# Kernel optimization log

Hardware: AMD Instinct MI355X
Metric: run time of the kernel (lower is better)

Reference implementation:

```python
import jax, jax.numpy as jnp
import numpy as np

BITS = 8
CLIP_BOUND = 2.0 ** (BITS - 1) - 1.0  # 127 for int8
EPS = 1e-12


def _per_tensor_scale(x):
    # Dynamic per-tensor abs-max calibration (TensorQuantizer.update with
    # calibration over the whole tensor): scale maps abs-max to the clip bound.
    amax = jnp.max(jnp.abs(x))
    return CLIP_BOUND / jnp.maximum(amax, EPS)


def setup_inputs() -> dict:
    key = jax.random.key(0)
    k1, k2 = jax.random.split(key)
    lhs = jax.random.normal(k1, (4096, 4096), dtype=jnp.float32)
    rhs = jax.random.normal(k2, (4096, 4096), dtype=jnp.float32)
    return {"lhs": lhs, "rhs": rhs}


def reference(lhs, rhs):
    # --- calibration (scales are statistics, no gradient flows through them) ---
    ls = _per_tensor_scale(lhs)
    rs = _per_tensor_scale(rhs)

    # --- quantize to int8 grid ---
    ql = jnp.clip(jnp.round(lhs * ls), -CLIP_BOUND, CLIP_BOUND).astype(jnp.int8)
    qr = jnp.clip(jnp.round(rhs * rs), -CLIP_BOUND, CLIP_BOUND).astype(jnp.int8)

    # --- integer dot_general with int32 accumulation (aqt_dot_general core) ---
    dimension_numbers = (((1,), (0,)), ((), ()))
    acc = jax.lax.dot_general(
        ql, qr, dimension_numbers, preferred_element_type=jnp.int32
    )

    # --- dequantize by product of scales ---
    out = acc.astype(jnp.float32) / (ls * rs)
    return out
```

## Files before the change

kernel.cpp:

```cpp
#include <hip/hip_runtime.h>
#include <stdint.h>


#define NROW 4096
#define NELEM (4096 * 4096)

typedef __attribute__((ext_vector_type(4))) int int32x4;
typedef __attribute__((ext_vector_type(16))) int int32x16;
typedef const __attribute__((address_space(1))) int8_t* gptr1_t;
typedef __attribute__((address_space(3))) int8_t* lptr3_t;

__global__ void absmax_both_kernel(const float* __restrict__ lhs,
                                   const float* __restrict__ rhs,
                                   unsigned* __restrict__ amax) {
    __shared__ float red[4];
    const int t = blockIdx.x & 1;
    const float4* x4 = (const float4*)(t ? rhs : lhs);
    const int bid = blockIdx.x >> 1;
    const int stride = (gridDim.x >> 1) * blockDim.x;
    int i = bid * blockDim.x + threadIdx.x;
    float m0 = 0.0f, m1 = 0.0f, m2 = 0.0f, m3 = 0.0f;
    for (; i + 3 * stride < NELEM / 4; i += 4 * stride) {
        float4 a = x4[i];
        float4 b = x4[i + stride];
        float4 c = x4[i + 2 * stride];
        float4 d = x4[i + 3 * stride];
        m0 = fmaxf(m0, fmaxf(fmaxf(fabsf(a.x), fabsf(a.y)),
                             fmaxf(fabsf(a.z), fabsf(a.w))));
        m1 = fmaxf(m1, fmaxf(fmaxf(fabsf(b.x), fabsf(b.y)),
                             fmaxf(fabsf(b.z), fabsf(b.w))));
        m2 = fmaxf(m2, fmaxf(fmaxf(fabsf(c.x), fabsf(c.y)),
                             fmaxf(fabsf(c.z), fabsf(c.w))));
        m3 = fmaxf(m3, fmaxf(fmaxf(fabsf(d.x), fabsf(d.y)),
                             fmaxf(fabsf(d.z), fabsf(d.w))));
    }
    for (; i < NELEM / 4; i += stride) {
        float4 a = x4[i];
        m0 = fmaxf(m0, fmaxf(fmaxf(fabsf(a.x), fabsf(a.y)),
                             fmaxf(fabsf(a.z), fabsf(a.w))));
    }
    float m = fmaxf(fmaxf(m0, m1), fmaxf(m2, m3));
    for (int off = 32; off > 0; off >>= 1)
        m = fmaxf(m, __shfl_down(m, off, 64));
    const int lane = threadIdx.x & 63, wave = threadIdx.x >> 6;
    if (lane == 0) red[wave] = m;
    __syncthreads();
    if (threadIdx.x == 0) {
        float b = fmaxf(fmaxf(red[0], red[1]), fmaxf(red[2], red[3]));
        atomicMax(amax + t, __float_as_uint(b));
    }
}

__device__ __forceinline__ int q8(float v, float s) {
    int r = __float2int_rn(v * s);
    r = r < -127 ? -127 : r;
    r = r > 127 ? 127 : r;
    return r;
}

__global__ void quant_kernel(const float* __restrict__ lhs,
                             const float* __restrict__ rhs,
                             int8_t* __restrict__ qA, int8_t* __restrict__ qT,
                             const unsigned* __restrict__ amax) {
    __shared__ int8_t sm[64][68];
    if (blockIdx.x < 16384) {
        const float s = 127.0f / fmaxf(__uint_as_float(amax[0]), 1e-12f);
        const int i = blockIdx.x * blockDim.x + threadIdx.x;
        float4 v = ((const float4*)lhs)[i];
        int b0 = q8(v.x, s), b1 = q8(v.y, s), b2 = q8(v.z, s), b3 = q8(v.w, s);
        ((int*)qA)[i] = (b0 & 0xff) | ((b1 & 0xff) << 8) | ((b2 & 0xff) << 16)
                      | ((b3 & 0xff) << 24);
    } else {
        const float s = 127.0f / fmaxf(__uint_as_float(amax[1]), 1e-12f);
        const int b = blockIdx.x - 16384;
        const int n0 = (b & 63) * 64, k0 = (b >> 6) * 64;
        const int rl = threadIdx.x >> 4;
        const int nq = threadIdx.x & 15;
        for (int r = 0; r < 4; ++r) {
            const int kl = r * 16 + rl;
            float4 v = *(const float4*)(rhs + (size_t)(k0 + kl) * NROW + n0 + nq * 4);
            sm[nq * 4 + 0][kl] = (int8_t)q8(v.x, s);
            sm[nq * 4 + 1][kl] = (int8_t)q8(v.y, s);
            sm[nq * 4 + 2][kl] = (int8_t)q8(v.z, s);
            sm[nq * 4 + 3][kl] = (int8_t)q8(v.w, s);
        }
        __syncthreads();
        const int nl = threadIdx.x >> 2;
        const int kq = threadIdx.x & 3;
        int4 w;
        w.x = *(const int*)&sm[nl][kq * 16 + 0];
        w.y = *(const int*)&sm[nl][kq * 16 + 4];
        w.z = *(const int*)&sm[nl][kq * 16 + 8];
        w.w = *(const int*)&sm[nl][kq * 16 + 12];
        *(int4*)(qT + (size_t)(n0 + nl) * NROW + k0 + kq * 16) = w;
    }
}

__global__ __launch_bounds__(512, 2) void gemm_i8_kernel(
    const int8_t* __restrict__ qA, const int8_t* __restrict__ qBT,
    float* __restrict__ out, const unsigned* __restrict__ amax) {
    __shared__ __align__(16) int8_t sA[2][256 * 128];
    __shared__ __align__(16) int8_t sB[2][256 * 128];

    const int tid = threadIdx.x;
    const int lane = tid & 63;
    const int wave = tid >> 6;
    const int wm = wave >> 2;
    const int wn = wave & 3;

    const int bid = blockIdx.y * 16 + blockIdx.x;
    const int swz = (bid & 7) * 32 + (bid >> 3);
    const int m0 = (swz >> 4) * 256, n0 = (swz & 15) * 256;

    const int rl = lane & 31;
    const int hi = lane >> 5;

    const int rowA = wm * 128 + rl;
    const int rowB = wn * 64 + rl;
    int aoff4[4], boff4[4];
#pragma unroll
    for (int ks = 0; ks < 4; ++ks) {
        aoff4[ks] = rowA * 128 + (((2 * ks + hi + rowA) & 7) << 4);
        boff4[ks] = rowB * 128 + (((2 * ks + hi + rowB) & 7) << 4);
    }

    gptr1_t pA[4], pB[4];
#pragma unroll
    for (int j = 0; j < 4; ++j) {
        const int c = tid + j * 512;
        const int row = c >> 3;
        const int G = ((c & 7) - row) & 7;
        pA[j] = (gptr1_t)(qA + (size_t)(m0 + row) * NROW + G * 16);
        pB[j] = (gptr1_t)(qBT + (size_t)(n0 + row) * NROW + G * 16);
    }
    int8_t* sAf = &sA[0][0];
    int8_t* sBf = &sB[0][0];
    const int dst0 = tid * 16;

    auto stage = [&](int slot, int kb) {
#pragma unroll
        for (int j = 0; j < 4; ++j) {
            __builtin_amdgcn_global_load_lds(
                pA[j] + kb, (lptr3_t)(sAf + slot * 32768 + dst0 + j * 8192),
                16, 0, 0);
            __builtin_amdgcn_global_load_lds(
                pB[j] + kb, (lptr3_t)(sBf + slot * 32768 + dst0 + j * 8192),
                16, 0, 0);
        }
    };

    int32x16 acc[4][2];
#pragma unroll
    for (int mt = 0; mt < 4; ++mt)
#pragma unroll
        for (int nt = 0; nt < 2; ++nt) acc[mt][nt] = (int32x16)(0);

    auto compute = [&](const int8_t* a, const int8_t* b) {
#pragma unroll
        for (int ks = 0; ks < 4; ++ks) {
            int32x4 af[4], bf[2];
#pragma unroll
            for (int mt = 0; mt < 4; ++mt)
                af[mt] = *(const int32x4*)(a + aoff4[ks] + mt * 4096);
#pragma unroll
            for (int nt = 0; nt < 2; ++nt)
                bf[nt] = *(const int32x4*)(b + boff4[ks] + nt * 4096);
            __builtin_amdgcn_s_setprio(1);
#pragma unroll
            for (int mt = 0; mt < 4; ++mt)
#pragma unroll
                for (int nt = 0; nt < 2; ++nt)
                    acc[mt][nt] = __builtin_amdgcn_mfma_i32_32x32x32_i8(
                        af[mt], bf[nt], acc[mt][nt], 0, 0, 0);
            __builtin_amdgcn_s_setprio(0);
        }
    };

    stage(0, 0);
    asm volatile("s_waitcnt vmcnt(0)" ::: "memory");
    __builtin_amdgcn_sched_barrier(0);
    __builtin_amdgcn_s_barrier();
    __builtin_amdgcn_sched_barrier(0);

#pragma unroll 1
    for (int w = 0; w < 31; ++w) {
        stage((w + 1) & 1, (w + 1) * 128);
        compute(sAf + (w & 1) * 32768, sBf + (w & 1) * 32768);
        asm volatile("s_waitcnt vmcnt(0)" ::: "memory");
        __builtin_amdgcn_sched_barrier(0);
        __builtin_amdgcn_s_barrier();
        __builtin_amdgcn_sched_barrier(0);
    }
    compute(sAf + 32768, sBf + 32768);

    const float ls = 127.0f / fmaxf(__uint_as_float(amax[0]), 1e-12f);
    const float rs = 127.0f / fmaxf(__uint_as_float(amax[1]), 1e-12f);
    const float inv = 1.0f / (ls * rs);
#pragma unroll
    for (int mt = 0; mt < 4; ++mt)
#pragma unroll
        for (int nt = 0; nt < 2; ++nt)
#pragma unroll
            for (int reg = 0; reg < 16; ++reg) {
                const int row = m0 + wm * 128 + mt * 32 + (reg & 3) +
                                8 * (reg >> 2) + 4 * hi;
                const int col = n0 + wn * 64 + nt * 32 + rl;
                out[(size_t)row * NROW + col] = (float)acc[mt][nt][reg] * inv;
            }
}

extern "C" void kernel_launch(void* const* d_in, const int* in_sizes, int n_in,
                              void* d_out, int out_size, void* d_ws,
                              size_t ws_size, hipStream_t stream) {
    const float* lhs = (const float*)d_in[0];
    const float* rhs = (const float*)d_in[1];
    float* out = (float*)d_out;

    int8_t* qA = (int8_t*)d_ws;
    int8_t* qBT = qA + (size_t)16 * 1024 * 1024;
    unsigned* amax = (unsigned*)(qBT + (size_t)16 * 1024 * 1024);

    hipMemsetAsync(amax, 0, 8, stream);
    absmax_both_kernel<<<2048, 256, 0, stream>>>(lhs, rhs, amax);
    quant_kernel<<<16384 + 4096, 256, 0, stream>>>(lhs, rhs, qA, qBT, amax);
    gemm_i8_kernel<<<dim3(16, 16), 512, 0, stream>>>(qA, qBT, out, amax);
}
```

Baseline: 141.0 us.

## Pre-pack int8 operands in MFMA fragment order and load GEMM operands directly from global

The quantize kernel now writes qA and qBT in a tiled layout matching the MFMA 32x32x32 fragment order, with each lane's 16 bytes contiguous. The GEMM drops the LDS staging, double buffer and block barriers, and loads fragments straight from global memory into registers with a two-deep register ping-pong. This removes LDS traffic and synchronisation, but gives up intra-block reuse through shared memory. Each wave now re-fetches A and B tiles that other waves also read, so the kernel leans on L2/cache and global load latency hiding.

```diff
diff --git a/kernel.cpp b/kernel.cpp
--- a/kernel.cpp
+++ b/kernel.cpp
@@ -7,8 +7,6 @@
 
 typedef __attribute__((ext_vector_type(4))) int int32x4;
 typedef __attribute__((ext_vector_type(16))) int int32x16;
-typedef const __attribute__((address_space(1))) int8_t* gptr1_t;
-typedef __attribute__((address_space(3))) int8_t* lptr3_t;
 
 __global__ void absmax_both_kernel(const float* __restrict__ lhs,
                                    const float* __restrict__ rhs,
@@ -58,21 +56,36 @@
     return r;
 }
 
+__device__ __forceinline__ int pack4(float a, float b, float c, float d,
+                                     float s) {
+    return (q8(a, s) & 0xff) | ((q8(b, s) & 0xff) << 8) |
+           ((q8(c, s) & 0xff) << 16) | ((q8(d, s) & 0xff) << 24);
+}
+
 __global__ void quant_kernel(const float* __restrict__ lhs,
                              const float* __restrict__ rhs,
                              int8_t* __restrict__ qA, int8_t* __restrict__ qT,
                              const unsigned* __restrict__ amax) {
     __shared__ int8_t sm[64][68];
-    if (blockIdx.x < 16384) {
+    if (blockIdx.x < 4096) {
         const float s = 127.0f / fmaxf(__uint_as_float(amax[0]), 1e-12f);
-        const int i = blockIdx.x * blockDim.x + threadIdx.x;
-        float4 v = ((const float4*)lhs)[i];
-        int b0 = q8(v.x, s), b1 = q8(v.y, s), b2 = q8(v.z, s), b3 = q8(v.w, s);
-        ((int*)qA)[i] = (b0 & 0xff) | ((b1 & 0xff) << 8) | ((b2 & 0xff) << 16)
-                      | ((b3 & 0xff) << 24);
+        const int c = blockIdx.x * 256 + threadIdx.x;
+        const int l = c & 63;
+        const int ks_g = (c >> 6) & 127;
+        const int mt_g = c >> 13;
+        const int row = mt_g * 32 + (l & 31);
+        const int kb = ks_g * 32 + (l >> 5) * 16;
+        const float4* src = (const float4*)(lhs + (size_t)row * NROW + kb);
+        float4 v0 = src[0], v1 = src[1], v2 = src[2], v3 = src[3];
+        int4 w;
+        w.x = pack4(v0.x, v0.y, v0.z, v0.w, s);
+        w.y = pack4(v1.x, v1.y, v1.z, v1.w, s);
+        w.z = pack4(v2.x, v2.y, v2.z, v2.w, s);
+        w.w = pack4(v3.x, v3.y, v3.z, v3.w, s);
+        *(int4*)(qA + (size_t)c * 16) = w;
     } else {
         const float s = 127.0f / fmaxf(__uint_as_float(amax[1]), 1e-12f);
-        const int b = blockIdx.x - 16384;
+        const int b = blockIdx.x - 4096;
         const int n0 = (b & 63) * 64, k0 = (b >> 6) * 64;
         const int rl = threadIdx.x >> 4;
         const int nq = threadIdx.x & 15;
@@ -85,23 +98,25 @@
             sm[nq * 4 + 3][kl] = (int8_t)q8(v.w, s);
         }
         __syncthreads();
-        const int nl = threadIdx.x >> 2;
-        const int kq = threadIdx.x & 3;
+        const int nt_l = threadIdx.x >> 7;
+        const int ks_l = (threadIdx.x >> 6) & 1;
+        const int l = threadIdx.x & 63;
+        const int n_loc = nt_l * 32 + (l & 31);
+        const int k_loc = ks_l * 32 + (l >> 5) * 16;
         int4 w;
-        w.x = *(const int*)&sm[nl][kq * 16 + 0];
-        w.y = *(const int*)&sm[nl][kq * 16 + 4];
-        w.z = *(const int*)&sm[nl][kq * 16 + 8];
-        w.w = *(const int*)&sm[nl][kq * 16 + 12];
-        *(int4*)(qT + (size_t)(n0 + nl) * NROW + k0 + kq * 16) = w;
+        w.x = *(const int*)&sm[n_loc][k_loc + 0];
+        w.y = *(const int*)&sm[n_loc][k_loc + 4];
+        w.z = *(const int*)&sm[n_loc][k_loc + 8];
+        w.w = *(const int*)&sm[n_loc][k_loc + 12];
+        const int nt_g = (b & 63) * 2 + nt_l;
+        const int ks_g = (b >> 6) * 2 + ks_l;
+        *(int4*)(qT + (((size_t)nt_g * 128 + ks_g) * 64 + l) * 16) = w;
     }
 }
 
 __global__ __launch_bounds__(512, 2) void gemm_i8_kernel(
     const int8_t* __restrict__ qA, const int8_t* __restrict__ qBT,
     float* __restrict__ out, const unsigned* __restrict__ amax) {
-    __shared__ __align__(16) int8_t sA[2][256 * 128];
-    __shared__ __align__(16) int8_t sB[2][256 * 128];
-
     const int tid = threadIdx.x;
     const int lane = tid & 63;
     const int wave = tid >> 6;
@@ -115,39 +130,8 @@
     const int rl = lane & 31;
     const int hi = lane >> 5;
 
-    const int rowA = wm * 128 + rl;
-    const int rowB = wn * 64 + rl;
-    int aoff4[4], boff4[4];
-#pragma unroll
-    for (int ks = 0; ks < 4; ++ks) {
-        aoff4[ks] = rowA * 128 + (((2 * ks + hi + rowA) & 7) << 4);
-        boff4[ks] = rowB * 128 + (((2 * ks + hi + rowB) & 7) << 4);
-    }
-
-    gptr1_t pA[4], pB[4];
-#pragma unroll
-    for (int j = 0; j < 4; ++j) {
-        const int c = tid + j * 512;
-        const int row = c >> 3;
-        const int G = ((c & 7) - row) & 7;
-        pA[j] = (gptr1_t)(qA + (size_t)(m0 + row) * NROW + G * 16);
-        pB[j] = (gptr1_t)(qBT + (size_t)(n0 + row) * NROW + G * 16);
-    }
-    int8_t* sAf = &sA[0][0];
-    int8_t* sBf = &sB[0][0];
-    const int dst0 = tid * 16;
-
-    auto stage = [&](int slot, int kb) {
-#pragma unroll
-        for (int j = 0; j < 4; ++j) {
-            __builtin_amdgcn_global_load_lds(
-                pA[j] + kb, (lptr3_t)(sAf + slot * 32768 + dst0 + j * 8192),
-                16, 0, 0);
-            __builtin_amdgcn_global_load_lds(
-                pB[j] + kb, (lptr3_t)(sBf + slot * 32768 + dst0 + j * 8192),
-                16, 0, 0);
-        }
-    };
+    const int8_t* pa = qA + ((size_t)(m0 / 32 + wm * 4) * 128 + 0) * 1024 + lane * 16;
+    const int8_t* pb = qBT + ((size_t)(n0 / 32 + wn * 2) * 128 + 0) * 1024 + lane * 16;
 
     int32x16 acc[4][2];
 #pragma unroll
@@ -155,43 +139,41 @@
 #pragma unroll
         for (int nt = 0; nt < 2; ++nt) acc[mt][nt] = (int32x16)(0);
 
-    auto compute = [&](const int8_t* a, const int8_t* b) {
-#pragma unroll
-        for (int ks = 0; ks < 4; ++ks) {
-            int32x4 af[4], bf[2];
-#pragma unroll
-            for (int mt = 0; mt < 4; ++mt)
-                af[mt] = *(const int32x4*)(a + aoff4[ks] + mt * 4096);
-#pragma unroll
-            for (int nt = 0; nt < 2; ++nt)
-                bf[nt] = *(const int32x4*)(b + boff4[ks] + nt * 4096);
-            __builtin_amdgcn_s_setprio(1);
-#pragma unroll
-            for (int mt = 0; mt < 4; ++mt)
-#pragma unroll
-                for (int nt = 0; nt < 2; ++nt)
-                    acc[mt][nt] = __builtin_amdgcn_mfma_i32_32x32x32_i8(
-                        af[mt], bf[nt], acc[mt][nt], 0, 0, 0);
-            __builtin_amdgcn_s_setprio(0);
-        }
-    };
-
-    stage(0, 0);
-    asm volatile("s_waitcnt vmcnt(0)" ::: "memory");
-    __builtin_amdgcn_sched_barrier(0);
-    __builtin_amdgcn_s_barrier();
-    __builtin_amdgcn_sched_barrier(0);
-
+    int32x4 a0[4], b0[2], a1[4], b1[2];
+
+#define LOADF(A, B, S)                                                        \
+    {                                                                         \
+        const int8_t* ap = pa + (S)*1024;                                     \
+        const int8_t* bp = pb + (S)*1024;                                     \
+        A[0] = *(const int32x4*)(ap);                                         \
+        A[1] = *(const int32x4*)(ap + 131072);                                \
+        A[2] = *(const int32x4*)(ap + 262144);                                \
+        A[3] = *(const int32x4*)(ap + 393216);                                \
+        B[0] = *(const int32x4*)(bp);                                         \
+        B[1] = *(const int32x4*)(bp + 131072);                                \
+    }
+
+#define MFMAF(A, B)                                                           \
+    {                                                                         \
+        __builtin_amdgcn_s_setprio(1);                                        \
+        _Pragma("unroll") for (int mt = 0; mt < 4; ++mt)                      \
+            _Pragma("unroll") for (int nt = 0; nt < 2; ++nt) acc[mt][nt] =    \
+                __builtin_amdgcn_mfma_i32_32x32x32_i8(A[mt], B[nt],           \
+                                                      acc[mt][nt], 0, 0, 0);  \
+        __builtin_amdgcn_s_setprio(0);                                        \
+    }
+
+    LOADF(a0, b0, 0)
 #pragma unroll 1
-    for (int w = 0; w < 31; ++w) {
-        stage((w + 1) & 1, (w + 1) * 128);
-        compute(sAf + (w & 1) * 32768, sBf + (w & 1) * 32768);
-        asm volatile("s_waitcnt vmcnt(0)" ::: "memory");
-        __builtin_amdgcn_sched_barrier(0);
-        __builtin_amdgcn_s_barrier();
-        __builtin_amdgcn_sched_barrier(0);
-    }
-    compute(sAf + 32768, sBf + 32768);
+    for (int s = 0; s < 126; s += 2) {
+        LOADF(a1, b1, s + 1)
+        MFMAF(a0, b0)
+        LOADF(a0, b0, s + 2)
+        MFMAF(a1, b1)
+    }
+    LOADF(a1, b1, 127)
+    MFMAF(a0, b0)
+    MFMAF(a1, b1)
 
     const float ls = 127.0f / fmaxf(__uint_as_float(amax[0]), 1e-12f);
     const float rs = 127.0f / fmaxf(__uint_as_float(amax[1]), 1e-12f);
@@ -207,6 +189,8 @@
                 const int col = n0 + wn * 64 + nt * 32 + rl;
                 out[(size_t)row * NROW + col] = (float)acc[mt][nt][reg] * inv;
             }
+#undef LOADF
+#undef MFMAF
 }
 
 extern "C" void kernel_launch(void* const* d_in, const int* in_sizes, int n_in,
@@ -222,6 +206,6 @@
 
     hipMemsetAsync(amax, 0, 8, stream);
     absmax_both_kernel<<<2048, 256, 0, stream>>>(lhs, rhs, amax);
-    quant_kernel<<<16384 + 4096, 256, 0, stream>>>(lhs, rhs, qA, qBT, amax);
+    quant_kernel<<<4096 + 4096, 256, 0, stream>>>(lhs, rhs, qA, qBT, amax);
     gemm_i8_kernel<<<dim3(16, 16), 512, 0, stream>>>(qA, qBT, out, amax);
 }
```

After: 142.4 us. Within noise of the previous version (+1.0%).
